# Kernel tuning notes

Measured on AMD Instinct MI355X. Metric: run time of the kernel, lower is better.

Reference implementation:

```python
import math
import jax, jax.numpy as jnp
import numpy as np

D, H, L, DFF, V = 512, 8, 6, 2048, 32000
B, S = 2, 2048
PAD = 1


def _layernorm(x, g, b, eps=1e-5):
    m = x.mean(-1, keepdims=True)
    v = ((x - m) ** 2).mean(-1, keepdims=True)
    return (x - m) / jnp.sqrt(v + eps) * g + b


def _mha(qx, kx, w, b, mask, h=H):
    # w: [4, D, D] (q,k,v,out), b: [4, D]; mask broadcastable to [B,1,Sq,Sk]
    bs, sq, d = qx.shape
    dk = d // h
    def proj(x, i):
        return (x @ w[i] + b[i]).reshape(bs, -1, h, dk).transpose(0, 2, 1, 3)
    q, k, v = proj(qx, 0), proj(kx, 1), proj(kx, 2)
    scores = jnp.einsum('bhqd,bhkd->bhqk', q, k) / math.sqrt(dk)
    scores = jnp.where(mask, scores, -jnp.inf)
    attn = jax.nn.softmax(scores, axis=-1)
    out = jnp.einsum('bhqk,bhkd->bhqd', attn, v).transpose(0, 2, 1, 3).reshape(bs, sq, d)
    return out @ w[3] + b[3]


def _ff(x, w1, b1, w2, b2):
    return jax.nn.relu(x @ w1 + b1) @ w2 + b2


def _sinusoidal_pe(max_len, d):
    pos = np.arange(max_len)[:, None].astype(np.float64)
    div = np.exp(np.arange(0, d, 2) * (-math.log(10000.0) / d))
    pe = np.zeros((max_len, d), np.float32)
    pe[:, 0::2] = np.sin(pos * div)
    pe[:, 1::2] = np.cos(pos * div)
    return jnp.asarray(pe[None])  # [1, max_len, d]


def setup_inputs() -> dict:
    key = jax.random.key(0)
    ks = iter(jax.random.split(key, 32))
    def w(shape):
        return jax.random.normal(next(ks), shape, jnp.float32) * 0.02
    inp = {
        'src': jax.random.randint(next(ks), (B, S), 2, V),
        'tgt': jax.random.randint(next(ks), (B, S), 2, V),
        'src_emb': w((V, D)),
        'tgt_emb': w((V, D)),
        'pe': _sinusoidal_pe(S, D),
        'enc_attn_w': w((L, 4, D, D)), 'enc_attn_b': jnp.zeros((L, 4, D)),
        'enc_ff_w1': w((L, D, DFF)), 'enc_ff_b1': jnp.zeros((L, DFF)),
        'enc_ff_w2': w((L, DFF, D)), 'enc_ff_b2': jnp.zeros((L, D)),
        'enc_ln_g': jnp.ones((L, 2, D)), 'enc_ln_b': jnp.zeros((L, 2, D)),
        'dec_self_w': w((L, 4, D, D)), 'dec_self_b': jnp.zeros((L, 4, D)),
        'dec_src_w': w((L, 4, D, D)), 'dec_src_b': jnp.zeros((L, 4, D)),
        'dec_ff_w1': w((L, D, DFF)), 'dec_ff_b1': jnp.zeros((L, DFF)),
        'dec_ff_w2': w((L, DFF, D)), 'dec_ff_b2': jnp.zeros((L, D)),
        'dec_ln_g': jnp.ones((L, 3, D)), 'dec_ln_b': jnp.zeros((L, 3, D)),
        'ln_g': jnp.ones((D,)), 'ln_b': jnp.zeros((D,)),
        'fc_w': w((D, V)), 'fc_b': jnp.zeros((V,)),
    }
    return inp


def reference(src, tgt, src_emb, tgt_emb, pe,
              enc_attn_w, enc_attn_b, enc_ff_w1, enc_ff_b1, enc_ff_w2, enc_ff_b2,
              enc_ln_g, enc_ln_b,
              dec_self_w, dec_self_b, dec_src_w, dec_src_b,
              dec_ff_w1, dec_ff_b1, dec_ff_w2, dec_ff_b2, dec_ln_g, dec_ln_b,
              ln_g, ln_b, fc_w, fc_b):
    s_len, t_len = src.shape[1], tgt.shape[1]
    src_mask = (src != PAD)[:, None, None, :]                      # [B,1,1,Ss]
    tril = jnp.tril(jnp.ones((t_len, t_len), bool))
    tgt_mask = (tgt != PAD)[:, None, None, :] & tril[None, None]   # [B,1,St,St]

    x = src_emb[src] + pe[:, :s_len]
    for l in range(L):
        x2 = _layernorm(x, enc_ln_g[l, 0], enc_ln_b[l, 0])
        x = x + _mha(x2, x2, enc_attn_w[l], enc_attn_b[l], src_mask)
        x2 = _layernorm(x, enc_ln_g[l, 1], enc_ln_b[l, 1])
        x = x + _ff(x2, enc_ff_w1[l], enc_ff_b1[l], enc_ff_w2[l], enc_ff_b2[l])
    memory = x

    y = tgt_emb[tgt] + pe[:, :t_len]
    for l in range(L):
        y2 = _layernorm(y, dec_ln_g[l, 0], dec_ln_b[l, 0])
        y = y + _mha(y2, y2, dec_self_w[l], dec_self_b[l], tgt_mask)
        y2 = _layernorm(y, dec_ln_g[l, 1], dec_ln_b[l, 1])
        y = y + _mha(y2, memory, dec_src_w[l], dec_src_b[l], src_mask)
        y2 = _layernorm(y, dec_ln_g[l, 2], dec_ln_b[l, 2])
        y = y + _ff(y2, dec_ff_w1[l], dec_ff_b1[l], dec_ff_w2[l], dec_ff_b2[l])

    return _layernorm(y, ln_g, ln_b) @ fc_w + fc_b  # [B, St, V]
```

## Files before the change

### kernel.cpp

```cpp
#include <hip/hip_runtime.h>
#include <math.h>

#define D_MODEL 512
#define NHEAD   8
#define NLAYER  6
#define DFF_    2048
#define VOCAB   32000
#define BATCH   2
#define SEQ     2048
#define NTOK    (BATCH*SEQ)
#define PAD_ID  1

typedef __attribute__((ext_vector_type(8))) short s16x8;
typedef __attribute__((ext_vector_type(4))) float f32x4;
typedef unsigned short u16;
typedef unsigned int   u32;
typedef unsigned long long u64;

__device__ __forceinline__ u16 f2bf(float x) {
  u32 u = __builtin_bit_cast(u32, x);
  u += 0x7FFFu + ((u >> 16) & 1u);
  return (u16)(u >> 16);
}

__device__ __forceinline__ float exp2i(float x) {
  float r; asm("v_exp_f32 %0, %1" : "=v"(r) : "v"(x)); return r;
}

__device__ __forceinline__ void gload16(const void* g, void* l) {
  __builtin_amdgcn_global_load_lds(
      (const __attribute__((address_space(1))) u32*)g,
      (__attribute__((address_space(3))) u32*)l, 16, 0, 0);
}

#define CEXP 0.1803368802f

__global__ __launch_bounds__(256) void embed2_kernel(
    const int* __restrict__ src, const int* __restrict__ tgt,
    const float* __restrict__ se, const float* __restrict__ te,
    const float* __restrict__ pe, float* __restrict__ xe, float* __restrict__ yd)
{
  const int z = blockIdx.y;
  const int* tok = z ? tgt : src;
  const float* emb = z ? te : se;
  float* out = z ? yd : xe;
  const int total = NTOK * D_MODEL;
  for (int i = blockIdx.x * 256 + threadIdx.x; i < total; i += gridDim.x * 256) {
    int t = i >> 9;
    int d = i & 511;
    int s = t & (SEQ - 1);
    out[i] = emb[(size_t)tok[t] * D_MODEL + d] + pe[(size_t)s * D_MODEL + d];
  }
}

__global__ __launch_bounds__(64) void padmask2_kernel(
    const int* __restrict__ src, const int* __restrict__ tgt,
    u64* __restrict__ pmS, u64* __restrict__ pmT)
{
  const int z = blockIdx.z;
  const int* tok = z ? tgt : src;
  u64* pm = z ? pmT : pmS;
  int b = blockIdx.y, t = blockIdx.x;
  int lane = threadIdx.x;
  u64 m = __ballot(tok[(size_t)b * SEQ + t * 64 + lane] != PAD_ID);
  if (lane == 0) pm[b * (SEQ / 64) + t] = m;
}

__global__ __launch_bounds__(256) void ln_kernel(
    const float* __restrict__ x, const float* __restrict__ g,
    const float* __restrict__ bb, u16* __restrict__ y)
{
  const int lane = threadIdx.x & 63;
  const size_t row = (size_t)blockIdx.x * 4 + (threadIdx.x >> 6);
  const float* xr = x + row * D_MODEL + lane * 8;
  float4 v0 = *(const float4*)xr;
  float4 v1 = *(const float4*)(xr + 4);
  float sum = (v0.x + v0.y) + (v0.z + v0.w) + (v1.x + v1.y) + (v1.z + v1.w);
  float ss = v0.x * v0.x + v0.y * v0.y + v0.z * v0.z + v0.w * v0.w
           + v1.x * v1.x + v1.y * v1.y + v1.z * v1.z + v1.w * v1.w;
  #pragma unroll
  for (int o = 1; o < 64; o <<= 1) {
    sum += __shfl_xor(sum, o, 64);
    ss  += __shfl_xor(ss, o, 64);
  }
  float mean = sum * (1.0f / D_MODEL);
  float inv = rsqrtf(ss * (1.0f / D_MODEL) - mean * mean + 1e-5f);
  float4 g0 = *(const float4*)&g[lane * 8];
  float4 g1 = *(const float4*)&g[lane * 8 + 4];
  float4 c0 = *(const float4*)&bb[lane * 8];
  float4 c1 = *(const float4*)&bb[lane * 8 + 4];
  uint4 o;
  o.x = (u32)f2bf((v0.x - mean) * inv * g0.x + c0.x) | ((u32)f2bf((v0.y - mean) * inv * g0.y + c0.y) << 16);
  o.y = (u32)f2bf((v0.z - mean) * inv * g0.z + c0.z) | ((u32)f2bf((v0.w - mean) * inv * g0.w + c0.w) << 16);
  o.z = (u32)f2bf((v1.x - mean) * inv * g1.x + c1.x) | ((u32)f2bf((v1.y - mean) * inv * g1.y + c1.y) << 16);
  o.w = (u32)f2bf((v1.z - mean) * inv * g1.z + c1.z) | ((u32)f2bf((v1.w - mean) * inv * g1.w + c1.w) << 16);
  *(uint4*)&y[row * D_MODEL + lane * 8] = o;
}

__global__ __launch_bounds__(256) void tconv2_kernel(
    const float* __restrict__ s0, const float* __restrict__ s1,
    u16* __restrict__ d0, u16* __restrict__ d1, int zsplit, int K, int N)
{
  __shared__ float tile[64][65];
  const int z = blockIdx.z;
  const float* src = (z < zsplit) ? s0 + (size_t)z * K * N : s1 + (size_t)(z - zsplit) * K * N;
  u16* dst = (z < zsplit) ? d0 + (size_t)z * K * N : d1 + (size_t)(z - zsplit) * K * N;
  const int n0 = blockIdx.x * 64, k0 = blockIdx.y * 64;
  const int t = threadIdx.x;
  const int cr = t >> 4, cc = (t & 15) * 4;
  #pragma unroll
  for (int it = 0; it < 4; ++it) {
    int kr = cr + it * 16;
    float4 v = *(const float4*)&src[(size_t)(k0 + kr) * N + n0 + cc];
    tile[kr][cc] = v.x; tile[kr][cc + 1] = v.y; tile[kr][cc + 2] = v.z; tile[kr][cc + 3] = v.w;
  }
  __syncthreads();
  #pragma unroll
  for (int it = 0; it < 4; ++it) {
    int nr = cr + it * 16;
    u32 lo = (u32)f2bf(tile[cc + 0][nr]) | ((u32)f2bf(tile[cc + 1][nr]) << 16);
    u32 hi = (u32)f2bf(tile[cc + 2][nr]) | ((u32)f2bf(tile[cc + 3][nr]) << 16);
    uint2 pk; pk.x = lo; pk.y = hi;
    *(uint2*)&dst[(size_t)(n0 + nr) * K + k0 + cc] = pk;
  }
}

__global__ __launch_bounds__(256) void tconv3_kernel(
    const float* __restrict__ s0, const float* __restrict__ s1,
    const float* __restrict__ s2, u16* __restrict__ dst0)
{
  __shared__ float tile[64][65];
  const int z = blockIdx.z;
  const float* src = (z < 24) ? s0 + (size_t)z * 262144
                   : (z < 48) ? s1 + (size_t)(z - 24) * 262144
                              : s2 + (size_t)(z - 48) * 262144;
  u16* dst = dst0 + (size_t)z * 262144;
  const int n0 = blockIdx.x * 64, k0 = blockIdx.y * 64;
  const int t = threadIdx.x;
  const int cr = t >> 4, cc = (t & 15) * 4;
  #pragma unroll
  for (int it = 0; it < 4; ++it) {
    int kr = cr + it * 16;
    float4 v = *(const float4*)&src[(size_t)(k0 + kr) * 512 + n0 + cc];
    tile[kr][cc] = v.x; tile[kr][cc + 1] = v.y; tile[kr][cc + 2] = v.z; tile[kr][cc + 3] = v.w;
  }
  __syncthreads();
  #pragma unroll
  for (int it = 0; it < 4; ++it) {
    int nr = cr + it * 16;
    u32 lo = (u32)f2bf(tile[cc + 0][nr]) | ((u32)f2bf(tile[cc + 1][nr]) << 16);
    u32 hi = (u32)f2bf(tile[cc + 2][nr]) | ((u32)f2bf(tile[cc + 3][nr]) << 16);
    uint2 pk; pk.x = lo; pk.y = hi;
    *(uint2*)&dst[(size_t)(n0 + nr) * 512 + k0 + cc] = pk;
  }
}

template<int MODE, int BM, int BN, int MAP>
__global__ __launch_bounds__(256, 2) void mm_kernel(
    const u16* __restrict__ A, const u16* __restrict__ Wt,
    const float* __restrict__ bias, const float* __restrict__ res,
    void* __restrict__ Cout, u16* __restrict__ vtOut,
    int M, int N, int K,
    long long wStride, long long bStride, long long cStride)
{
  constexpr int MI = BM / 32;
  constexpr int NI = BN / 32;
  constexpr bool DB = (BM == 64 && BN == 64);
  __shared__ u16 sh[(DB ? 2 : 1) * (BM + BN) * 64];
  const int z = blockIdx.z;
  size_t wOff, bOff;
  if (MAP == 1) {
    wOff = (size_t)(z >> 1) * 4 * 262144 + (size_t)(1 + (z & 1)) * 262144;
    bOff = (size_t)(z >> 1) * 4 * 512 + (size_t)(1 + (z & 1)) * 512;
  } else {
    wOff = (size_t)z * wStride;
    bOff = (size_t)z * bStride;
  }
  Wt += wOff;
  bias += bOff;
  const int bm = blockIdx.y * BM, bn = blockIdx.x * BN;
  const int tid = threadIdx.x, lane = tid & 63, w = tid >> 6;
  const int wm = w >> 1, wn = w & 1;
  const int l15 = lane & 15, l4 = lane >> 4;
  const int wrow0 = wm * (BM / 2), wcol0 = wn * (BN / 2);
  const u16* aBase = A  + (size_t)bm * K;
  const u16* bBase = Wt + (size_t)bn * K;
  f32x4 acc[MI][NI] = {};

  auto mfma_step = [&](const u16* Asb, const u16* Bsb) {
    #pragma unroll
    for (int ks = 0; ks < 2; ++ks) {
      s16x8 af[MI], bf[NI];
      #pragma unroll
      for (int mi = 0; mi < MI; ++mi) {
        int rr = wrow0 + mi * 16 + l15;
        af[mi] = *(const s16x8*)&Asb[(rr << 6) + (((ks * 4 + l4) ^ (rr & 7)) << 3)];
      }
      #pragma unroll
      for (int ni = 0; ni < NI; ++ni) {
        int rr = wcol0 + ni * 16 + l15;
        bf[ni] = *(const s16x8*)&Bsb[(rr << 6) + (((ks * 4 + l4) ^ (rr & 7)) << 3)];
      }
      #pragma unroll
      for (int mi = 0; mi < MI; ++mi)
        #pragma unroll
        for (int ni = 0; ni < NI; ++ni)
          acc[mi][ni] = __builtin_amdgcn_mfma_f32_16x16x32_bf16(af[mi], bf[ni], acc[mi][ni], 0, 0, 0);
    }
  };

  if constexpr (DB) {
    u16* As0 = sh;
    u16* As1 = sh + 64 * 64;
    u16* Bs0 = sh + 2 * 64 * 64;
    u16* Bs1 = sh + 3 * 64 * 64;
    auto stage = [&](int k0, u16* Ad, u16* Bd) {
      #pragma unroll
      for (int i = 0; i < 2; ++i) {
        int lin = i * 256 + tid;
        int r = lin >> 3, sp = lin & 7;
        gload16(aBase + (size_t)r * K + k0 + ((sp ^ (r & 7)) * 8), &Ad[(i * 256 + w * 64) * 8]);
      }
      #pragma unroll
      for (int i = 0; i < 2; ++i) {
        int lin = i * 256 + tid;
        int r = lin >> 3, sp = lin & 7;
        gload16(bBase + (size_t)r * K + k0 + ((sp ^ (r & 7)) * 8), &Bd[(i * 256 + w * 64) * 8]);
      }
    };
    stage(0, As0, Bs0);
    __syncthreads();
    const int nt = K >> 6;
    for (int t = 0; t < nt; ++t) {
      const bool even = !(t & 1);
      u16* Ac = even ? As0 : As1;
      u16* Bc = even ? Bs0 : Bs1;
      if (t + 1 < nt) stage((t + 1) << 6, even ? As1 : As0, even ? Bs1 : Bs0);
      mfma_step(Ac, Bc);
      __syncthreads();
    }
  } else {
    u16* As = sh;
    u16* Bs = sh + BM * 64;
    for (int k0 = 0; k0 < K; k0 += 64) {
      #pragma unroll
      for (int i = 0; i < BM / 32; ++i) {
        int lin = i * 256 + tid;
        int r = lin >> 3, sp = lin & 7;
        gload16(aBase + (size_t)r * K + k0 + ((sp ^ (r & 7)) * 8), &As[(i * 256 + w * 64) * 8]);
      }
      #pragma unroll
      for (int i = 0; i < BN / 32; ++i) {
        int lin = i * 256 + tid;
        int r = lin >> 3, sp = lin & 7;
        gload16(bBase + (size_t)r * K + k0 + ((sp ^ (r & 7)) * 8), &Bs[(i * 256 + w * 64) * 8]);
      }
      __syncthreads();
      mfma_step(As, Bs);
      __syncthreads();
    }
  }

  const bool vpath = (MODE == 4 && z == 2) || (MODE == 5 && (z & 1) == 1);
  if (vpath) {
    u16* TT = sh;
    #pragma unroll
    for (int mi = 0; mi < MI; ++mi)
      #pragma unroll
      for (int ni = 0; ni < NI; ++ni)
        #pragma unroll
        for (int r = 0; r < 4; ++r) {
          int rowl = wrow0 + mi * 16 + l4 * 4 + r;
          int coll = wcol0 + ni * 16 + l15;
          TT[coll * 72 + rowl] = f2bf(acc[mi][ni][r] + bias[bn + coll]);
        }
    __syncthreads();
    const int b = bm >> 11, s0loc = bm & 2047, h = bn >> 6;
    const int layer = (MODE == 5) ? (z >> 1) : 0;
    u16* vbase = vtOut + (size_t)layer * ((size_t)NTOK * D_MODEL)
               + ((size_t)(b * NHEAD + h) * 64) * SEQ;
    int d = tid >> 2, sc = (tid & 3) * 16;
    s16x8 v0 = *(const s16x8*)&TT[d * 72 + sc];
    s16x8 v1 = *(const s16x8*)&TT[d * 72 + sc + 8];
    *(s16x8*)(vbase + (size_t)d * SEQ + s0loc + sc) = v0;
    *(s16x8*)(vbase + (size_t)d * SEQ + s0loc + sc + 8) = v1;
    return;
  }

  const int zi = (MAP == 1) ? (z >> 1) : z;
  #pragma unroll
  for (int ni = 0; ni < NI; ++ni) {
    int col = bn + wcol0 + ni * 16 + l15;
    float bb = bias[col];
    #pragma unroll
    for (int mi = 0; mi < MI; ++mi) {
      #pragma unroll
      for (int r = 0; r < 4; ++r) {
        int row = bm + wrow0 + mi * 16 + l4 * 4 + r;
        size_t off = (size_t)zi * cStride + (size_t)row * N + col;
        float v = acc[mi][ni][r] + bb;
        if (MODE == 1 || MODE == 6) v += res[(size_t)row * N + col];
        if (MODE == 3) v = fmaxf(v, 0.0f);
        if (MODE <= 1 || MODE == 6) ((float*)Cout)[off] = v;
        else                        ((u16*)Cout)[off] = f2bf(v);
        if (MODE == 6) vtOut[(size_t)row * N + col] = f2bf(v);
      }
    }
  }
}

template<int CAUSAL, int QPROJ>
__global__ __launch_bounds__(256, 2) void fattn_kernel(
    const u16* __restrict__ Qg, const u16* __restrict__ Kg,
    const u16* __restrict__ Vt, const u16* __restrict__ Wq,
    const float* __restrict__ qbias, const u64* __restrict__ padm,
    u16* __restrict__ Og)
{
  __shared__ u16 Ks[2][128 * 64];
  __shared__ u16 Vs[2][64 * 128];
  __shared__ u16 Ps[4][16 * 128];
  const int qtile = CAUSAL ? (int)(gridDim.x - 1 - blockIdx.x) : (int)blockIdx.x;
  const int qt = qtile * 64;
  const int h = blockIdx.y, b = blockIdx.z;
  const int tid = threadIdx.x, lane = tid & 63, w = tid >> 6;
  const int l15 = lane & 15, l4 = lane >> 4;
  const int hoff = h * 64;
  const u16* Kbase = Kg + (size_t)(b * SEQ) * D_MODEL + hoff;
  const u16* Vbase = Vt + (size_t)(b * NHEAD + h) * 64 * SEQ;
  const u64* pmb = padm + b * (SEQ / 64);
  const int qg = qt + w * 16 + l15;

  s16x8 aq[2];
  if constexpr (QPROJ) {
    const u16* xBase = Qg + (size_t)(b * SEQ + qt) * D_MODEL;
    const u16* wBase = Wq + (size_t)hoff * D_MODEL;
    u16* Xs = Ks[0];
    u16* Wsh = Ks[0] + 64 * 64;
    f32x4 qa[4] = {};
    for (int k0 = 0; k0 < 512; k0 += 64) {
      #pragma unroll
      for (int i = 0; i < 2; ++i) {
        int lin = i * 256 + tid;
        int r = lin >> 3, sp = lin & 7;
        gload16(xBase + (size_t)r * D_MODEL + k0 + ((sp ^ (r & 7)) * 8), &Xs[(i * 256 + w * 64) * 8]);
      }
      #pragma unroll
      for (int i = 0; i < 2; ++i) {
        int lin = i * 256 + tid;
        int r = lin >> 3, sp = lin & 7;
        gload16(wBase + (size_t)r * D_MODEL + k0 + ((sp ^ (r & 7)) * 8), &Wsh[(i * 256 + w * 64) * 8]);
      }
      __syncthreads();
      #pragma unroll
      for (int ks = 0; ks < 2; ++ks) {
        int rr = w * 16 + l15;
        s16x8 xa = *(const s16x8*)&Xs[(rr << 6) + (((ks * 4 + l4) ^ (rr & 7)) << 3)];
        #pragma unroll
        for (int ni = 0; ni < 4; ++ni) {
          int rw = ni * 16 + l15;
          s16x8 wb = *(const s16x8*)&Wsh[(rw << 6) + (((ks * 4 + l4) ^ (rw & 7)) << 3)];
          qa[ni] = __builtin_amdgcn_mfma_f32_16x16x32_bf16(xa, wb, qa[ni], 0, 0, 0);
        }
      }
      __syncthreads();
    }
    u16* Qsh = (u16*)Ps;
    #pragma unroll
    for (int ni = 0; ni < 4; ++ni) {
      int col = ni * 16 + l15;
      float bb = qbias[hoff + col];
      #pragma unroll
      for (int r = 0; r < 4; ++r) {
        int row = w * 16 + l4 * 4 + r;
        Qsh[(row << 6) + ((((col >> 3)) ^ (row & 7)) << 3) + (col & 7)] = f2bf(qa[ni][r] + bb);
      }
    }
    __syncthreads();
    {
      int rr = w * 16 + l15;
      aq[0] = *(const s16x8*)&Qsh[(rr << 6) + (((0 + l4) ^ (rr & 7)) << 3)];
      aq[1] = *(const s16x8*)&Qsh[(rr << 6) + (((4 + l4) ^ (rr & 7)) << 3)];
    }
  } else {
    const u16* qp = Qg + (size_t)(b * SEQ + qg) * D_MODEL + hoff + l4 * 8;
    aq[0] = *(const s16x8*)qp;
    aq[1] = *(const s16x8*)(qp + 32);
  }

  f32x4 oacc[4] = {};
  float mrow = -1e30f, lrow = 0.f;
  const int nt = CAUSAL ? (qt >> 7) + 1 : SEQ / 128;

  #define STAGE(KV0, BUF)                                                              \
    {                                                                                  \
      _Pragma("unroll")                                                                \
      for (int it = 0; it < 4; ++it) {                                                 \
        int lin = it * 256 + tid;                                                      \
        int rr = lin >> 3, sp = lin & 7;                                               \
        gload16(Kbase + (size_t)((KV0) + rr) * D_MODEL + ((sp ^ (rr & 7)) * 8),        \
                &Ks[BUF][(it * 256 + w * 64) * 8]);                                    \
      }                                                                                \
      _Pragma("unroll")                                                                \
      for (int it = 0; it < 4; ++it) {                                                 \
        int lin = it * 256 + tid;                                                      \
        int rr = lin >> 4, ko = lin & 15;                                              \
        gload16(Vbase + (size_t)rr * SEQ + (KV0) + ((ko ^ (rr & 15)) * 8),             \
                &Vs[BUF][(it * 256 + w * 64) * 8]);                                    \
      }                                                                                \
    }

  if constexpr (QPROJ) __syncthreads();
  STAGE(0, 0);
  __syncthreads();

  for (int kt = 0; kt < nt; ++kt) {
    const int kv0 = kt * 128;
    const int cur = kt & 1;
    if (kt + 1 < nt) STAGE(kv0 + 128, cur ^ 1);

    f32x4 sac[8] = {};
    #pragma unroll
    for (int ks = 0; ks < 2; ++ks)
      #pragma unroll
      for (int jn = 0; jn < 8; ++jn) {
        int rr = jn * 16 + l15;
        s16x8 ak = *(const s16x8*)&Ks[cur][(rr << 6) + (((ks * 4 + l4) ^ (rr & 7)) << 3)];
        sac[jn] = __builtin_amdgcn_mfma_f32_16x16x32_bf16(ak, aq[ks], sac[jn], 0, 0, 0);
      }

    const u64 m0 = pmb[(kv0 >> 6)];
    const u64 m1 = pmb[(kv0 >> 6) + 1];
    const bool lastC = CAUSAL && (kt == nt - 1);
    if (((m0 & m1) != ~0ull) || lastC) {
      #pragma unroll
      for (int jn = 0; jn < 8; ++jn) {
        u64 mm = (jn < 4) ? m0 : m1;
        #pragma unroll
        for (int r = 0; r < 4; ++r) {
          int kl = (jn & 3) * 16 + l4 * 4 + r;
          int kvg = kv0 + jn * 16 + l4 * 4 + r;
          bool ok = ((mm >> kl) & 1) && (!CAUSAL || kvg <= qg);
          if (!ok) sac[jn][r] = -1e30f;
        }
      }
    }

    float m = sac[0][0];
    #pragma unroll
    for (int jn = 0; jn < 8; ++jn)
      #pragma unroll
      for (int r = 0; r < 4; ++r) m = fmaxf(m, sac[jn][r]);
    m = fmaxf(m, __shfl_xor(m, 16, 64));
    m = fmaxf(m, __shfl_xor(m, 32, 64));

    if (__any(m - mrow > 64.0f)) {
      float mn = fmaxf(mrow, m);
      float sc = exp2i((mrow - mn) * CEXP);
      mrow = mn;
      lrow *= sc;
      #pragma unroll
      for (int jn = 0; jn < 4; ++jn)
        #pragma unroll
        for (int r = 0; r < 4; ++r) oacc[jn][r] *= sc;
    }

    float rs = 0.f;
    #pragma unroll
    for (int jn = 0; jn < 8; ++jn) {
      float p0 = exp2i((sac[jn][0] - mrow) * CEXP);
      float p1 = exp2i((sac[jn][1] - mrow) * CEXP);
      float p2 = exp2i((sac[jn][2] - mrow) * CEXP);
      float p3 = exp2i((sac[jn][3] - mrow) * CEXP);
      rs += (p0 + p1) + (p2 + p3);
      uint2 pk;
      pk.x = (u32)f2bf(p0) | ((u32)f2bf(p1) << 16);
      pk.y = (u32)f2bf(p2) | ((u32)f2bf(p3) << 16);
      int pu = (jn * 4 + l4) ^ ((l15 & 7) << 2);
      *(uint2*)&Ps[w][l15 * 128 + pu * 4] = pk;
    }
    rs += __shfl_xor(rs, 16, 64);
    rs += __shfl_xor(rs, 32, 64);
    lrow += rs;

    #pragma unroll
    for (int ks2 = 0; ks2 < 4; ++ks2) {
      int pu = (ks2 * 8 + l4 * 2) ^ ((l15 & 7) << 2);
      s16x8 pb = *(const s16x8*)&Ps[w][l15 * 128 + pu * 4];
      #pragma unroll
      for (int jn = 0; jn < 4; ++jn) {
        int rr = jn * 16 + l15;
        s16x8 av = *(const s16x8*)&Vs[cur][(rr << 7) + (((ks2 * 4 + l4) ^ (rr & 15)) << 3)];
        oacc[jn] = __builtin_amdgcn_mfma_f32_16x16x32_bf16(av, pb, oacc[jn], 0, 0, 0);
      }
    }
    __syncthreads();
  }
  #undef STAGE

  const float inv = 1.0f / lrow;
  u16* orow = Og + (size_t)(b * SEQ + qg) * D_MODEL + hoff;
  #pragma unroll
  for (int jn = 0; jn < 4; ++jn) {
    uint2 pk;
    pk.x = (u32)f2bf(oacc[jn][0] * inv) | ((u32)f2bf(oacc[jn][1] * inv) << 16);
    pk.y = (u32)f2bf(oacc[jn][2] * inv) | ((u32)f2bf(oacc[jn][3] * inv) << 16);
    *(uint2*)(orow + jn * 16 + l4 * 4) = pk;
  }
}

extern "C" void kernel_launch(void* const* d_in, const int* in_sizes, int n_in,
                              void* d_out, int out_size, void* d_ws, size_t ws_size,
                              hipStream_t stream)
{
  const int*   src        = (const int*)  d_in[0];
  const int*   tgt        = (const int*)  d_in[1];
  const float* src_emb    = (const float*)d_in[2];
  const float* tgt_emb    = (const float*)d_in[3];
  const float* pe         = (const float*)d_in[4];
  const float* enc_attn_w = (const float*)d_in[5];
  const float* enc_attn_b = (const float*)d_in[6];
  const float* enc_ff_w1  = (const float*)d_in[7];
  const float* enc_ff_b1  = (const float*)d_in[8];
  const float* enc_ff_w2  = (const float*)d_in[9];
  const float* enc_ff_b2  = (const float*)d_in[10];
  const float* enc_ln_g   = (const float*)d_in[11];
  const float* enc_ln_bb  = (const float*)d_in[12];
  const float* dec_self_w = (const float*)d_in[13];
  const float* dec_self_b = (const float*)d_in[14];
  const float* dec_src_w  = (const float*)d_in[15];
  const float* dec_src_b  = (const float*)d_in[16];
  const float* dec_ff_w1  = (const float*)d_in[17];
  const float* dec_ff_b1  = (const float*)d_in[18];
  const float* dec_ff_w2  = (const float*)d_in[19];
  const float* dec_ff_b2  = (const float*)d_in[20];
  const float* dec_ln_g   = (const float*)d_in[21];
  const float* dec_ln_bb  = (const float*)d_in[22];
  const float* fin_ln_g   = (const float*)d_in[23];
  const float* fin_ln_b   = (const float*)d_in[24];
  const float* fc_w       = (const float*)d_in[25];
  const float* fc_b       = (const float*)d_in[26];
  float* out = (float*)d_out;

  const size_t DD = (size_t)D_MODEL * D_MODEL;
  const size_t FD = (size_t)D_MODEL * DFF_;
  const size_t TD = (size_t)NTOK * D_MODEL;

  char* ob = (char*)d_out;
  size_t off = 0;
  auto alloco = [&](size_t bytes) { void* p = ob + off; off += (bytes + 255) & ~(size_t)255; return p; };
  u16* wt_enc_attn = (u16*)alloco(24 * DD * 2);
  u16* wt_dec_self = (u16*)alloco(24 * DD * 2);
  u16* wt_dec_src  = (u16*)alloco(24 * DD * 2);
  u16* wt_enc_ff1  = (u16*)alloco(6 * FD * 2);
  u16* wt_enc_ff2  = (u16*)alloco(6 * FD * 2);
  u16* wt_dec_ff1  = (u16*)alloco(6 * FD * 2);
  u16* wt_dec_ff2  = (u16*)alloco(6 * FD * 2);
  u16* qb   = (u16*)alloco(2 * TD * 2);
  u16* kb   = qb + TD;
  u16* vtb  = (u16*)alloco(TD * 2);
  u16* aob  = (u16*)alloco(TD * 2);
  u16* hbb  = (u16*)alloco((size_t)NTOK * DFF_ * 2);
  u16* memb = (u16*)alloco(TD * 2);
  u16* ckb  = (u16*)alloco(6 * TD * 2);
  u16* cvtb = (u16*)alloco(6 * TD * 2);

  char* wsb = (char*)d_ws;
  u16*   fcwt = (u16*)wsb;
  size_t wo = ((size_t)VOCAB * D_MODEL * 2 + 255) & ~(size_t)255;
  float* xe  = (float*)(wsb + wo); wo += TD * 4;
  float* yd  = (float*)(wsb + wo); wo += TD * 4;
  u16*   x2b = (u16*)(wsb + wo);   wo += TD * 2;
  u64*   pmS = (u64*)(wsb + wo);   wo += 1024;
  u64*   pmT = (u64*)(wsb + wo);

  dim3 blk(256);
  dim3 gN512(8, 64, 1), gQKV(8, 64, 3), gCKV(8, 64, 12);
  dim3 gFF1(16, 32, 1), gFC(125, 32, 1);
  dim3 gAttn(SEQ / 64, NHEAD, BATCH);
  dim3 gLN(NTOK / 4);
  const long long llDD = (long long)DD, llTD = (long long)TD;

  padmask2_kernel<<<dim3(SEQ / 64, BATCH, 2), dim3(64), 0, stream>>>(src, tgt, pmS, pmT);
  tconv3_kernel<<<dim3(8, 8, 72), blk, 0, stream>>>(enc_attn_w, dec_self_w, dec_src_w, wt_enc_attn);
  tconv2_kernel<<<dim3(32, 8, 12), blk, 0, stream>>>(enc_ff_w1, dec_ff_w1, wt_enc_ff1, wt_dec_ff1, 6, 512, 2048);
  tconv2_kernel<<<dim3(8, 32, 12), blk, 0, stream>>>(enc_ff_w2, dec_ff_w2, wt_enc_ff2, wt_dec_ff2, 6, 2048, 512);
  tconv2_kernel<<<dim3(500, 8, 1), blk, 0, stream>>>(fc_w, fc_w, fcwt, fcwt, 1, 512, VOCAB);
  embed2_kernel<<<dim3(2048, 2), blk, 0, stream>>>(src, tgt, src_emb, tgt_emb, pe, xe, yd);

  for (int l = 0; l < NLAYER; ++l) {
    ln_kernel<<<gLN, blk, 0, stream>>>(xe, enc_ln_g + (size_t)(l * 2 + 0) * D_MODEL,
                                       enc_ln_bb + (size_t)(l * 2 + 0) * D_MODEL, x2b);
    mm_kernel<4, 64, 64, 0><<<gQKV, blk, 0, stream>>>(x2b, wt_enc_attn + (size_t)l * 4 * DD,
        enc_attn_b + (size_t)l * 4 * D_MODEL, nullptr, qb, vtb, NTOK, 512, 512, llDD, D_MODEL, llTD);
    fattn_kernel<0, 0><<<gAttn, blk, 0, stream>>>(qb, kb, vtb, nullptr, nullptr, pmS, aob);
    mm_kernel<1, 64, 64, 0><<<gN512, blk, 0, stream>>>(aob, wt_enc_attn + (size_t)(l * 4 + 3) * DD,
        enc_attn_b + (size_t)(l * 4 + 3) * D_MODEL, xe, xe, nullptr, NTOK, 512, 512, 0, 0, 0);
    ln_kernel<<<gLN, blk, 0, stream>>>(xe, enc_ln_g + (size_t)(l * 2 + 1) * D_MODEL,
                                       enc_ln_bb + (size_t)(l * 2 + 1) * D_MODEL, x2b);
    mm_kernel<3, 128, 128, 0><<<gFF1, blk, 0, stream>>>(x2b, wt_enc_ff1 + (size_t)l * FD,
        enc_ff_b1 + (size_t)l * DFF_, nullptr, hbb, nullptr, NTOK, DFF_, 512, 0, 0, 0);
    if (l == NLAYER - 1)
      mm_kernel<6, 64, 64, 0><<<gN512, blk, 0, stream>>>(hbb, wt_enc_ff2 + (size_t)l * FD,
          enc_ff_b2 + (size_t)l * D_MODEL, xe, xe, memb, NTOK, 512, DFF_, 0, 0, 0);
    else
      mm_kernel<1, 64, 64, 0><<<gN512, blk, 0, stream>>>(hbb, wt_enc_ff2 + (size_t)l * FD,
          enc_ff_b2 + (size_t)l * D_MODEL, xe, xe, nullptr, NTOK, 512, DFF_, 0, 0, 0);
  }

  mm_kernel<5, 64, 64, 1><<<gCKV, blk, 0, stream>>>(memb, wt_dec_src, dec_src_b, nullptr,
      ckb, cvtb, NTOK, 512, 512, 0, 0, llTD);

  for (int l = 0; l < NLAYER; ++l) {
    const u16* Ws = wt_dec_self + (size_t)l * 4 * DD;
    const u16* Wc = wt_dec_src + (size_t)l * 4 * DD;
    const float* bs  = dec_self_b + (size_t)l * 4 * D_MODEL;
    const float* bcb = dec_src_b + (size_t)l * 4 * D_MODEL;
    ln_kernel<<<gLN, blk, 0, stream>>>(yd, dec_ln_g + (size_t)(l * 3 + 0) * D_MODEL,
                                       dec_ln_bb + (size_t)(l * 3 + 0) * D_MODEL, x2b);
    mm_kernel<4, 64, 64, 0><<<gQKV, blk, 0, stream>>>(x2b, Ws, bs, nullptr, qb, vtb,
                                                      NTOK, 512, 512, llDD, D_MODEL, llTD);
    fattn_kernel<1, 0><<<gAttn, blk, 0, stream>>>(qb, kb, vtb, nullptr, nullptr, pmT, aob);
    mm_kernel<1, 64, 64, 0><<<gN512, blk, 0, stream>>>(aob, Ws + 3 * DD, bs + 3 * D_MODEL, yd, yd,
                                                       nullptr, NTOK, 512, 512, 0, 0, 0);
    ln_kernel<<<gLN, blk, 0, stream>>>(yd, dec_ln_g + (size_t)(l * 3 + 1) * D_MODEL,
                                       dec_ln_bb + (size_t)(l * 3 + 1) * D_MODEL, x2b);
    fattn_kernel<0, 1><<<gAttn, blk, 0, stream>>>(x2b, ckb + (size_t)l * TD, cvtb + (size_t)l * TD,
                                                  Wc, bcb, pmS, aob);
    mm_kernel<1, 64, 64, 0><<<gN512, blk, 0, stream>>>(aob, Wc + 3 * DD, bcb + 3 * D_MODEL, yd, yd,
                                                       nullptr, NTOK, 512, 512, 0, 0, 0);
    ln_kernel<<<gLN, blk, 0, stream>>>(yd, dec_ln_g + (size_t)(l * 3 + 2) * D_MODEL,
                                       dec_ln_bb + (size_t)(l * 3 + 2) * D_MODEL, x2b);
    mm_kernel<3, 128, 128, 0><<<gFF1, blk, 0, stream>>>(x2b, wt_dec_ff1 + (size_t)l * FD,
        dec_ff_b1 + (size_t)l * DFF_, nullptr, hbb, nullptr, NTOK, DFF_, 512, 0, 0, 0);
    mm_kernel<1, 64, 64, 0><<<gN512, blk, 0, stream>>>(hbb, wt_dec_ff2 + (size_t)l * FD,
        dec_ff_b2 + (size_t)l * D_MODEL, yd, yd, nullptr, NTOK, 512, DFF_, 0, 0, 0);
  }

  ln_kernel<<<gLN, blk, 0, stream>>>(yd, fin_ln_g, fin_ln_b, x2b);
  mm_kernel<0, 128, 256, 0><<<gFC, blk, 0, stream>>>(x2b, fcwt, fc_b, nullptr, out, nullptr,
                                                     NTOK, VOCAB, 512, 0, 0, 0);

  (void)in_sizes; (void)n_in; (void)out_size; (void)ws_size;
}
```

Baseline: 2.285 ms.

## Double-buffer square GEMM tiles, enlarge attention query tile, swap FC grid order

Three separate changes. Square GEMM tiles (including the 128x128 FF1 kernel) now use double-buffered shared memory, so loads overlap MFMA work. The flash-attention kernel moves to 512 threads and 128-query tiles, which halves the number of K/V tile loads per query and spreads staging across more threads. The vocab projection grid is transposed with an XSWAP template flag, so consecutive blocks share the same weight tile for L2 reuse. Risks include the larger LDS footprint for the 128x128 double buffer, which lowers occupancy, and fewer attention blocks, which lowers parallelism; the attention body also has to cope correctly with 8 waves.

```diff
diff --git a/kernel.cpp b/kernel.cpp
--- a/kernel.cpp
+++ b/kernel.cpp
@@ -155,7 +155,7 @@
   }
 }
 
-template<int MODE, int BM, int BN, int MAP>
+template<int MODE, int BM, int BN, int MAP, int XSWAP = 0>
 __global__ __launch_bounds__(256, 2) void mm_kernel(
     const u16* __restrict__ A, const u16* __restrict__ Wt,
     const float* __restrict__ bias, const float* __restrict__ res,
@@ -165,7 +165,7 @@
 {
   constexpr int MI = BM / 32;
   constexpr int NI = BN / 32;
-  constexpr bool DB = (BM == 64 && BN == 64);
+  constexpr bool DB = (BM == BN);
   __shared__ u16 sh[(DB ? 2 : 1) * (BM + BN) * 64];
   const int z = blockIdx.z;
   size_t wOff, bOff;
@@ -178,7 +178,8 @@
   }
   Wt += wOff;
   bias += bOff;
-  const int bm = blockIdx.y * BM, bn = blockIdx.x * BN;
+  const int bm = (XSWAP ? blockIdx.x : blockIdx.y) * BM;
+  const int bn = (XSWAP ? blockIdx.y : blockIdx.x) * BN;
   const int tid = threadIdx.x, lane = tid & 63, w = tid >> 6;
   const int wm = w >> 1, wn = w & 1;
   const int l15 = lane & 15, l4 = lane >> 4;
@@ -211,18 +212,18 @@
 
   if constexpr (DB) {
     u16* As0 = sh;
-    u16* As1 = sh + 64 * 64;
-    u16* Bs0 = sh + 2 * 64 * 64;
-    u16* Bs1 = sh + 3 * 64 * 64;
+    u16* As1 = sh + BM * 64;
+    u16* Bs0 = sh + 2 * BM * 64;
+    u16* Bs1 = sh + 2 * BM * 64 + BN * 64;
     auto stage = [&](int k0, u16* Ad, u16* Bd) {
       #pragma unroll
-      for (int i = 0; i < 2; ++i) {
+      for (int i = 0; i < BM / 32; ++i) {
         int lin = i * 256 + tid;
         int r = lin >> 3, sp = lin & 7;
         gload16(aBase + (size_t)r * K + k0 + ((sp ^ (r & 7)) * 8), &Ad[(i * 256 + w * 64) * 8]);
       }
       #pragma unroll
-      for (int i = 0; i < 2; ++i) {
+      for (int i = 0; i < BN / 32; ++i) {
         int lin = i * 256 + tid;
         int r = lin >> 3, sp = lin & 7;
         gload16(bBase + (size_t)r * K + k0 + ((sp ^ (r & 7)) * 8), &Bd[(i * 256 + w * 64) * 8]);
@@ -310,7 +311,7 @@
 }
 
 template<int CAUSAL, int QPROJ>
-__global__ __launch_bounds__(256, 2) void fattn_kernel(
+__global__ __launch_bounds__(512, 2) void fattn_kernel(
     const u16* __restrict__ Qg, const u16* __restrict__ Kg,
     const u16* __restrict__ Vt, const u16* __restrict__ Wq,
     const float* __restrict__ qbias, const u64* __restrict__ padm,
@@ -318,9 +319,9 @@
 {
   __shared__ u16 Ks[2][128 * 64];
   __shared__ u16 Vs[2][64 * 128];
-  __shared__ u16 Ps[4][16 * 128];
+  __shared__ u16 Ps[8][16 * 128];
   const int qtile = CAUSAL ? (int)(gridDim.x - 1 - blockIdx.x) : (int)blockIdx.x;
-  const int qt = qtile * 64;
+  const int qt = qtile * 128;
   const int h = blockIdx.y, b = blockIdx.z;
   const int tid = threadIdx.x, lane = tid & 63, w = tid >> 6;
   const int l15 = lane & 15, l4 = lane >> 4;
@@ -334,21 +335,19 @@
   if constexpr (QPROJ) {
     const u16* xBase = Qg + (size_t)(b * SEQ + qt) * D_MODEL;
     const u16* wBase = Wq + (size_t)hoff * D_MODEL;
-    u16* Xs = Ks[0];
-    u16* Wsh = Ks[0] + 64 * 64;
+    u16* Xs  = Ks[0];
+    u16* Wsh = Vs[0];
     f32x4 qa[4] = {};
     for (int k0 = 0; k0 < 512; k0 += 64) {
       #pragma unroll
       for (int i = 0; i < 2; ++i) {
-        int lin = i * 256 + tid;
+        int lin = i * 512 + tid;
         int r = lin >> 3, sp = lin & 7;
-        gload16(xBase + (size_t)r * D_MODEL + k0 + ((sp ^ (r & 7)) * 8), &Xs[(i * 256 + w * 64) * 8]);
-      }
-      #pragma unroll
-      for (int i = 0; i < 2; ++i) {
-        int lin = i * 256 + tid;
-        int r = lin >> 3, sp = lin & 7;
-        gload16(wBase + (size_t)r * D_MODEL + k0 + ((sp ^ (r & 7)) * 8), &Wsh[(i * 256 + w * 64) * 8]);
+        gload16(xBase + (size_t)r * D_MODEL + k0 + ((sp ^ (r & 7)) * 8), &Xs[(i * 512 + w * 64) * 8]);
+      }
+      {
+        int r = tid >> 3, sp = tid & 7;
+        gload16(wBase + (size_t)r * D_MODEL + k0 + ((sp ^ (r & 7)) * 8), &Wsh[(w * 64) * 8]);
       }
       __syncthreads();
       #pragma unroll
@@ -394,18 +393,18 @@
   #define STAGE(KV0, BUF)                                                              \
     {                                                                                  \
       _Pragma("unroll")                                                                \
-      for (int it = 0; it < 4; ++it) {                                                 \
-        int lin = it * 256 + tid;                                                      \
+      for (int it = 0; it < 2; ++it) {                                                 \
+        int lin = it * 512 + tid;                                                      \
         int rr = lin >> 3, sp = lin & 7;                                               \
         gload16(Kbase + (size_t)((KV0) + rr) * D_MODEL + ((sp ^ (rr & 7)) * 8),        \
-                &Ks[BUF][(it * 256 + w * 64) * 8]);                                    \
+                &Ks[BUF][(it * 512 + w * 64) * 8]);                                    \
       }                                                                                \
       _Pragma("unroll")                                                                \
-      for (int it = 0; it < 4; ++it) {                                                 \
-        int lin = it * 256 + tid;                                                      \
+      for (int it = 0; it < 2; ++it) {                                                 \
+        int lin = it * 512 + tid;                                                      \
         int rr = lin >> 4, ko = lin & 15;                                              \
         gload16(Vbase + (size_t)rr * SEQ + (KV0) + ((ko ^ (rr & 15)) * 8),             \
-                &Vs[BUF][(it * 256 + w * 64) * 8]);                                    \
+                &Vs[BUF][(it * 512 + w * 64) * 8]);                                    \
       }                                                                                \
     }
 
@@ -573,10 +572,10 @@
   u64*   pmS = (u64*)(wsb + wo);   wo += 1024;
   u64*   pmT = (u64*)(wsb + wo);
 
-  dim3 blk(256);
+  dim3 blk(256), blkA(512);
   dim3 gN512(8, 64, 1), gQKV(8, 64, 3), gCKV(8, 64, 12);
-  dim3 gFF1(16, 32, 1), gFC(125, 32, 1);
-  dim3 gAttn(SEQ / 64, NHEAD, BATCH);
+  dim3 gFF1(16, 32, 1), gFC(32, 125, 1);
+  dim3 gAttn(SEQ / 128, NHEAD, BATCH);
   dim3 gLN(NTOK / 4);
   const long long llDD = (long long)DD, llTD = (long long)TD;
 
@@ -592,7 +591,7 @@
                                        enc_ln_bb + (size_t)(l * 2 + 0) * D_MODEL, x2b);
     mm_kernel<4, 64, 64, 0><<<gQKV, blk, 0, stream>>>(x2b, wt_enc_attn + (size_t)l * 4 * DD,
         enc_attn_b + (size_t)l * 4 * D_MODEL, nullptr, qb, vtb, NTOK, 512, 512, llDD, D_MODEL, llTD);
-    fattn_kernel<0, 0><<<gAttn, blk, 0, stream>>>(qb, kb, vtb, nullptr, nullptr, pmS, aob);
+    fattn_kernel<0, 0><<<gAttn, blkA, 0, stream>>>(qb, kb, vtb, nullptr, nullptr, pmS, aob);
     mm_kernel<1, 64, 64, 0><<<gN512, blk, 0, stream>>>(aob, wt_enc_attn + (size_t)(l * 4 + 3) * DD,
         enc_attn_b + (size_t)(l * 4 + 3) * D_MODEL, xe, xe, nullptr, NTOK, 512, 512, 0, 0, 0);
     ln_kernel<<<gLN, blk, 0, stream>>>(xe, enc_ln_g + (size_t)(l * 2 + 1) * D_MODEL,
@@ -619,13 +618,13 @@
                                        dec_ln_bb + (size_t)(l * 3 + 0) * D_MODEL, x2b);
     mm_kernel<4, 64, 64, 0><<<gQKV, blk, 0, stream>>>(x2b, Ws, bs, nullptr, qb, vtb,
                                                       NTOK, 512, 512, llDD, D_MODEL, llTD);
-    fattn_kernel<1, 0><<<gAttn, blk, 0, stream>>>(qb, kb, vtb, nullptr, nullptr, pmT, aob);
+    fattn_kernel<1, 0><<<gAttn, blkA, 0, stream>>>(qb, kb, vtb, nullptr, nullptr, pmT, aob);
     mm_kernel<1, 64, 64, 0><<<gN512, blk, 0, stream>>>(aob, Ws + 3 * DD, bs + 3 * D_MODEL, yd, yd,
                                                        nullptr, NTOK, 512, 512, 0, 0, 0);
     ln_kernel<<<gLN, blk, 0, stream>>>(yd, dec_ln_g + (size_t)(l * 3 + 1) * D_MODEL,
                                        dec_ln_bb + (size_t)(l * 3 + 1) * D_MODEL, x2b);
-    fattn_kernel<0, 1><<<gAttn, blk, 0, stream>>>(x2b, ckb + (size_t)l * TD, cvtb + (size_t)l * TD,
-                                                  Wc, bcb, pmS, aob);
+    fattn_kernel<0, 1><<<gAttn, blkA, 0, stream>>>(x2b, ckb + (size_t)l * TD, cvtb + (size_t)l * TD,
+                                                   Wc, bcb, pmS, aob);
     mm_kernel<1, 64, 64, 0><<<gN512, blk, 0, stream>>>(aob, Wc + 3 * DD, bcb + 3 * D_MODEL, yd, yd,
                                                        nullptr, NTOK, 512, 512, 0, 0, 0);
     ln_kernel<<<gLN, blk, 0, stream>>>(yd, dec_ln_g + (size_t)(l * 3 + 2) * D_MODEL,
@@ -637,8 +636,8 @@
   }
 
   ln_kernel<<<gLN, blk, 0, stream>>>(yd, fin_ln_g, fin_ln_b, x2b);
-  mm_kernel<0, 128, 256, 0><<<gFC, blk, 0, stream>>>(x2b, fcwt, fc_b, nullptr, out, nullptr,
-                                                     NTOK, VOCAB, 512, 0, 0, 0);
+  mm_kernel<0, 128, 256, 0, 1><<<gFC, blk, 0, stream>>>(x2b, fcwt, fc_b, nullptr, out, nullptr,
+                                                        NTOK, VOCAB, 512, 0, 0, 0);
 
   (void)in_sizes; (void)n_in; (void)out_size; (void)ws_size;
 }
```

Result: no change. 2.274 ms (-0.4%).
